# Performance work log

Measured on AMD Instinct MI355X. Metric: run time of the kernel, lower is better.

The kernel has to match this reference:

```python
import jax, jax.numpy as jnp
import numpy as np
from jax import lax

DIM = 256
NUM_HEADS = 8
HEAD_DIM = DIM // NUM_HEADS          # 32
KEY_DIM = int(HEAD_DIM * 0.5)        # 16
SCALE = KEY_DIM ** -0.5
H_QKV = DIM + KEY_DIM * NUM_HEADS * 2  # 512
BN_EPS = 1e-3  # keras BatchNormalization default epsilon


def conv_bn(x, w, gamma, beta, mean, var, groups=1):
    # Conv2D (no bias) + BatchNorm (inference), activation=None
    y = lax.conv_general_dilated(
        x, w, window_strides=(1, 1), padding='SAME',
        dimension_numbers=('NHWC', 'HWIO', 'NHWC'),
        feature_group_count=groups)
    return gamma * (y - mean) * lax.rsqrt(var + BN_EPS) + beta


def setup_inputs() -> dict:
    key = jax.random.key(0)
    ks = jax.random.split(key, 4)
    B, Hs, Ws = 8, 32, 32
    inp = {
        'inputs': jax.random.normal(ks[0], (B, Hs, Ws, DIM), dtype=jnp.float32),
        # qkv: 1x1 conv dim -> h
        'qkv_w': jax.random.normal(ks[1], (1, 1, DIM, H_QKV), dtype=jnp.float32) * 0.05,
        'qkv_gamma': jnp.ones((H_QKV,), jnp.float32),
        'qkv_beta': jnp.zeros((H_QKV,), jnp.float32),
        'qkv_mean': jnp.zeros((H_QKV,), jnp.float32),
        'qkv_var': jnp.ones((H_QKV,), jnp.float32),
        # pe: 3x3 depthwise conv (groups=dim)
        'pe_w': jax.random.normal(ks[2], (3, 3, 1, DIM), dtype=jnp.float32) * 0.05,
        'pe_gamma': jnp.ones((DIM,), jnp.float32),
        'pe_beta': jnp.zeros((DIM,), jnp.float32),
        'pe_mean': jnp.zeros((DIM,), jnp.float32),
        'pe_var': jnp.ones((DIM,), jnp.float32),
        # proj: 1x1 conv dim -> dim
        'proj_w': jax.random.normal(ks[3], (1, 1, DIM, DIM), dtype=jnp.float32) * 0.05,
        'proj_gamma': jnp.ones((DIM,), jnp.float32),
        'proj_beta': jnp.zeros((DIM,), jnp.float32),
        'proj_mean': jnp.zeros((DIM,), jnp.float32),
        'proj_var': jnp.ones((DIM,), jnp.float32),
    }
    return inp


def reference(inputs, qkv_w, qkv_gamma, qkv_beta, qkv_mean, qkv_var,
              pe_w, pe_gamma, pe_beta, pe_mean, pe_var,
              proj_w, proj_gamma, proj_beta, proj_mean, proj_var):
    B, Hs, Ws, C = inputs.shape
    N = Hs * Ws
    x = conv_bn(inputs, qkv_w, qkv_gamma, qkv_beta, qkv_mean, qkv_var)  # [B,H,W,h]
    x = x.reshape(B, N, NUM_HEADS, 2 * KEY_DIM + HEAD_DIM)
    q = x[..., :KEY_DIM]                          # [B,N,nh,kd]
    k = x[..., KEY_DIM:2 * KEY_DIM]               # [B,N,nh,kd]
    v = x[..., 2 * KEY_DIM:]                      # [B,N,nh,hd]
    # attn = q^T @ k^T : [B,nh,N,N]
    attn = jnp.einsum('bnhk,bmhk->bhnm', q, k) * SCALE
    attn = jax.nn.softmax(attn, axis=-1)
    # x = v^T @ attn : [B,nh,hd,N]
    x = jnp.einsum('bnhd,bhnm->bhdm', v, attn)
    # faithful to source: transpose [0,2,1,3] -> [B,hd,nh,N], then reshape NHWC
    x = jnp.transpose(x, (0, 2, 1, 3)).reshape(B, Hs, Ws, C)
    pe = conv_bn(v.reshape(B, Hs, Ws, C), pe_w, pe_gamma, pe_beta, pe_mean, pe_var, groups=C)
    x = x + pe
    x = conv_bn(x, proj_w, proj_gamma, proj_beta, proj_mean, proj_var)
    return x
```

## Files before the change

### kernel.cpp

```cpp
#include <hip/hip_runtime.h>

typedef _Float16 h4 __attribute__((ext_vector_type(4)));
typedef _Float16 h8 __attribute__((ext_vector_type(8)));
typedef float    f4 __attribute__((ext_vector_type(4)));

#define QSCALE (0.25f * 1.44269504088896f)

__device__ __forceinline__ float ex2(float x){ return __builtin_amdgcn_exp2f(x); }

__global__ __launch_bounds__(256) void prep_k(
    const float* __restrict__ X,
    const float* __restrict__ qkvw, const float* __restrict__ qg, const float* __restrict__ qb,
    const float* __restrict__ qm,   const float* __restrict__ qv,
    const float* __restrict__ pew,  const float* __restrict__ pg, const float* __restrict__ pb,
    const float* __restrict__ pm,   const float* __restrict__ pv,
    const float* __restrict__ prw,  const float* __restrict__ prg, const float* __restrict__ prb,
    const float* __restrict__ prm,  const float* __restrict__ prv,
    _Float16* __restrict__ Xh, _Float16* __restrict__ Wqkv, float* __restrict__ bqkv,
    _Float16* __restrict__ Wproj, float* __restrict__ bproj,
    float* __restrict__ peW, float* __restrict__ peB)
{
  const int gid = blockIdx.x*256 + threadIdx.x;
  const int gsz = gridDim.x*256;
  for (int i = gid; i < 2097152/4; i += gsz){
    const float4 xv = ((const float4*)X)[i];
    h4 o; o[0]=(_Float16)xv.x; o[1]=(_Float16)xv.y; o[2]=(_Float16)xv.z; o[3]=(_Float16)xv.w;
    ((h4*)Xh)[i] = o;
  }
  for (int i = gid; i < 512*256; i += gsz){
    int o = i >> 8, c = i & 255;
    float s = qg[o] * rsqrtf(qv[o] + 1e-3f);
    Wqkv[i] = (_Float16)(qkvw[c*512 + o] * s);
  }
  for (int i = gid; i < 512; i += gsz){
    float s = qg[i] * rsqrtf(qv[i] + 1e-3f);
    bqkv[i] = qb[i] - qm[i]*s;
  }
  for (int i = gid; i < 256*256; i += gsz){
    int o = i >> 8, c = i & 255;
    float s = prg[o] * rsqrtf(prv[o] + 1e-3f);
    Wproj[i] = (_Float16)(prw[c*256 + o] * s);
  }
  for (int i = gid; i < 256; i += gsz){
    float s = prg[i] * rsqrtf(prv[i] + 1e-3f);
    bproj[i] = prb[i] - prm[i]*s;
  }
  for (int i = gid; i < 9*256; i += gsz){
    int c = i & 255;
    float s = pg[c] * rsqrtf(pv[c] + 1e-3f);
    peW[i] = pew[i] * s;
  }
  for (int i = gid; i < 256; i += gsz){
    float s = pg[i] * rsqrtf(pv[i] + 1e-3f);
    peB[i] = pb[i] - pm[i]*s;
  }
}

template<int EPI, int MT>
__global__ __launch_bounds__(256) void gemm_k(
    const _Float16* __restrict__ A, const _Float16* __restrict__ Bt,
    const float* __restrict__ bias,
    _Float16* __restrict__ Qh, _Float16* __restrict__ Kh, _Float16* __restrict__ Vh,
    float* __restrict__ Out)
{
  const int t = threadIdx.x, lane = t & 63, wv = t >> 6;
  const int l15 = lane & 15, q = lane >> 4;
  const int mb = (blockIdx.x*4 + wv) * (16*MT);
  const int n0 = blockIdx.y * 64;
  f4 acc[MT][4] = {};
  #pragma unroll
  for (int kk = 0; kk < 8; ++kk){
    h8 af[MT];
    #pragma unroll
    for (int mi = 0; mi < MT; ++mi)
      af[mi] = *(const h8*)(A + (size_t)(mb + mi*16 + l15)*256 + kk*32 + q*8);
    #pragma unroll
    for (int nj = 0; nj < 4; ++nj){
      h8 bf = *(const h8*)(Bt + (size_t)(n0 + nj*16 + l15)*256 + kk*32 + q*8);
      #pragma unroll
      for (int mi = 0; mi < MT; ++mi)
        acc[mi][nj] = __builtin_amdgcn_mfma_f32_16x16x32_f16(af[mi], bf, acc[mi][nj], 0,0,0);
    }
  }
  #pragma unroll
  for (int mi = 0; mi < MT; ++mi)
  #pragma unroll
  for (int nj = 0; nj < 4; ++nj){
    const int og = n0 + nj*16 + l15;
    const float bs = bias[og];
    #pragma unroll
    for (int r = 0; r < 4; ++r){
      const int mg = mb + mi*16 + q*4 + r;
      const float v = acc[mi][nj][r] + bs;
      if (EPI == 0){
        const int h = og >> 6, j = og & 63;
        const int b = mg >> 10, n = mg & 1023;
        const size_t bhn = (size_t)(b*8+h)*1024 + n;
        if (j < 16)      Qh[bhn*16 + j]      = (_Float16)(v * QSCALE);
        else if (j < 32) Kh[bhn*16 + (j-16)] = (_Float16)v;
        else             Vh[bhn*32 + (j-32)] = (_Float16)v;
      } else {
        Out[(size_t)mg*256 + og] = v;
      }
    }
  }
}

__global__ __launch_bounds__(256) void pass1_k(
    const _Float16* __restrict__ Qh, const _Float16* __restrict__ Kh,
    const _Float16* __restrict__ Vh, _Float16* __restrict__ Vs)
{
  const int t = threadIdx.x, lane = t & 63, wv = t >> 6;
  const int l15 = lane & 15, q = lane >> 4;
  const int bh = blockIdx.y;
  const int n0 = (blockIdx.x*4 + wv) * 32;
  const size_t qb = (size_t)bh*1024;
  const h4 af0 = *(const h4*)(Qh + (qb + n0 + l15)*16 + q*4);
  const h4 af1 = *(const h4*)(Qh + (qb + n0 + 16 + l15)*16 + q*4);
  f4 sm0 = {0.f,0.f,0.f,0.f}, sm1 = {0.f,0.f,0.f,0.f};
  const _Float16* kp = Kh + qb*16;
  #pragma unroll 4
  for (int mt = 0; mt < 64; ++mt){
    h4 bf = *(const h4*)(kp + mt*256 + l15*16 + q*4);
    f4 z = {0.f,0.f,0.f,0.f};
    f4 d0 = __builtin_amdgcn_mfma_f32_16x16x16f16(af0, bf, z, 0,0,0);
    f4 d1 = __builtin_amdgcn_mfma_f32_16x16x16f16(af1, bf, z, 0,0,0);
    #pragma unroll
    for (int r = 0; r < 4; ++r){ sm0[r] += ex2(d0[r]); sm1[r] += ex2(d1[r]); }
  }
  #pragma unroll
  for (int st = 1; st < 16; st <<= 1){
    #pragma unroll
    for (int r = 0; r < 4; ++r){
      sm0[r] += __shfl_xor(sm0[r], st, 64);
      sm1[r] += __shfl_xor(sm1[r], st, 64);
    }
  }
  f4 cv0, cv1;
  #pragma unroll
  for (int r = 0; r < 4; ++r){ cv0[r] = 1.0f/sm0[r]; cv1[r] = 1.0f/sm1[r]; }
  #pragma unroll
  for (int half = 0; half < 2; ++half){
    const int dd = l15 + half*16;
    h4 o0, o1;
    #pragma unroll
    for (int r = 0; r < 4; ++r){
      o0[r] = (_Float16)((float)Vh[(qb + n0 + q*4 + r)*32 + dd] * cv0[r]);
      o1[r] = (_Float16)((float)Vh[(qb + n0 + 16 + q*4 + r)*32 + dd] * cv1[r]);
    }
    *(h4*)(Vs + ((size_t)bh*32 + dd)*1024 + n0 + q*4)      = o0;
    *(h4*)(Vs + ((size_t)bh*32 + dd)*1024 + n0 + 16 + q*4) = o1;
  }
}

__global__ __launch_bounds__(256) void pass2_k(
    const _Float16* __restrict__ Qh, const _Float16* __restrict__ Kh,
    const _Float16* __restrict__ Vs, _Float16* __restrict__ X1h)
{
  __shared__ float Tt[4][32*33];
  const int t = threadIdx.x, lane = t & 63, wv = t >> 6;
  const int l15 = lane & 15, q = lane >> 4;
  const int bh = blockIdx.y;
  const int b  = bh >> 3, h = bh & 7;
  const int mb = (blockIdx.x*4 + wv) * 32;
  const size_t qb = (size_t)bh*1024;
  const h4 kf0 = *(const h4*)(Kh + (qb + mb + l15)*16 + q*4);
  const h4 kf1 = *(const h4*)(Kh + (qb + mb + 16 + l15)*16 + q*4);
  const _Float16* qp  = Qh + qb*16;
  const _Float16* vp0 = Vs + ((size_t)bh*32 + l15)*1024;
  const _Float16* vp1 = vp0 + 16*1024;
  f4 a00={0.f,0.f,0.f,0.f}, a01={0.f,0.f,0.f,0.f};
  f4 a10={0.f,0.f,0.f,0.f}, a11={0.f,0.f,0.f,0.f};
  #pragma unroll 2
  for (int nt = 0; nt < 1024; nt += 16){
    h4 qf = *(const h4*)(qp + (nt + l15)*16 + q*4);
    h4 b0 = *(const h4*)(vp0 + nt + q*4);
    h4 b1 = *(const h4*)(vp1 + nt + q*4);
    f4 z = {0.f,0.f,0.f,0.f};
    f4 s0 = __builtin_amdgcn_mfma_f32_16x16x16f16(qf, kf0, z, 0,0,0);
    f4 s1 = __builtin_amdgcn_mfma_f32_16x16x16f16(qf, kf1, z, 0,0,0);
    h4 p0, p1;
    #pragma unroll
    for (int r = 0; r < 4; ++r){ p0[r] = (_Float16)ex2(s0[r]); p1[r] = (_Float16)ex2(s1[r]); }
    a00 = __builtin_amdgcn_mfma_f32_16x16x16f16(p0, b0, a00, 0,0,0);
    a01 = __builtin_amdgcn_mfma_f32_16x16x16f16(p0, b1, a01, 0,0,0);
    a10 = __builtin_amdgcn_mfma_f32_16x16x16f16(p1, b0, a10, 0,0,0);
    a11 = __builtin_amdgcn_mfma_f32_16x16x16f16(p1, b1, a11, 0,0,0);
  }
  #pragma unroll
  for (int r = 0; r < 4; ++r){
    Tt[wv][(q*4 + r)*33      + l15]      = a00[r];
    Tt[wv][(q*4 + r)*33      + 16 + l15] = a01[r];
    Tt[wv][(16 + q*4 + r)*33 + l15]      = a10[r];
    Tt[wv][(16 + q*4 + r)*33 + 16 + l15] = a11[r];
  }
  __syncthreads();
  _Float16* xb = X1h + (size_t)b*262144 + (size_t)h*1024 + mb;
  const int mloc = lane & 31, dh = lane >> 5;
  #pragma unroll
  for (int r = 0; r < 16; ++r){
    const int d = r*2 + dh;
    xb[(size_t)d*8192 + mloc] = (_Float16)Tt[wv][mloc*33 + d];
  }
}

__global__ __launch_bounds__(256) void pe_add_k(
    const _Float16* __restrict__ Vh, const _Float16* __restrict__ X1h,
    const float* __restrict__ peW, const float* __restrict__ peB,
    _Float16* __restrict__ X2h)
{
  const int idx = blockIdx.x*256 + threadIdx.x;
  const int c = idx & 255;
  const int tok = idx >> 8;
  const int b = tok >> 10, n = tok & 1023;
  const int hs = n >> 5, ws = n & 31;
  const int h = c >> 5, d = c & 31;
  float acc = peB[c];
  const _Float16* vb = Vh + (size_t)(b*8 + h)*32768 + d;
  #pragma unroll
  for (int dy = 0; dy < 3; ++dy){
    const int y = hs + dy - 1;
    if ((unsigned)y < 32u){
      #pragma unroll
      for (int dx = 0; dx < 3; ++dx){
        const int x = ws + dx - 1;
        if ((unsigned)x < 32u)
          acc += peW[(dy*3+dx)*256 + c] * (float)vb[(size_t)(y*32 + x)*32];
      }
    }
  }
  X2h[idx] = (_Float16)((float)X1h[idx] + acc);
}

extern "C" void kernel_launch(void* const* d_in, const int* in_sizes, int n_in,
                              void* d_out, int out_size, void* d_ws, size_t ws_size,
                              hipStream_t stream)
{
  const float* X    = (const float*)d_in[0];
  const float* qkvw = (const float*)d_in[1];
  const float* qg   = (const float*)d_in[2];
  const float* qb   = (const float*)d_in[3];
  const float* qm   = (const float*)d_in[4];
  const float* qv   = (const float*)d_in[5];
  const float* pew  = (const float*)d_in[6];
  const float* pg   = (const float*)d_in[7];
  const float* pb   = (const float*)d_in[8];
  const float* pm   = (const float*)d_in[9];
  const float* pv   = (const float*)d_in[10];
  const float* prw  = (const float*)d_in[11];
  const float* prg  = (const float*)d_in[12];
  const float* prb  = (const float*)d_in[13];
  const float* prm  = (const float*)d_in[14];
  const float* prv  = (const float*)d_in[15];

  char* ws = (char*)d_ws;
  _Float16* Xh    = (_Float16*)(ws + 0);
  _Float16* X2h   = (_Float16*)(ws + 0);
  _Float16* Qh    = (_Float16*)(ws + 4194304);
  _Float16* Kh    = (_Float16*)(ws + 6291456);
  _Float16* Vh    = (_Float16*)(ws + 8388608);
  _Float16* Vs    = (_Float16*)(ws + 12582912);
  _Float16* X1h   = (_Float16*)(ws + 16777216);
  _Float16* Wqkv  = (_Float16*)(ws + 20971520);
  float*    bqkv  = (float*)   (ws + 21233664);
  _Float16* Wproj = (_Float16*)(ws + 21235712);
  float*    bproj = (float*)   (ws + 21366784);
  float*    peW   = (float*)   (ws + 21367808);
  float*    peB   = (float*)   (ws + 21377024);

  prep_k<<<256, 256, 0, stream>>>(X, qkvw, qg, qb, qm, qv, pew, pg, pb, pm, pv,
                                  prw, prg, prb, prm, prv,
                                  Xh, Wqkv, bqkv, Wproj, bproj, peW, peB);
  gemm_k<0,2><<<dim3(64, 8), 256, 0, stream>>>(Xh, Wqkv, bqkv, Qh, Kh, Vh, nullptr);
  pass1_k<<<dim3(8, 64), 256, 0, stream>>>(Qh, Kh, Vh, Vs);
  pass2_k<<<dim3(8, 64), 256, 0, stream>>>(Qh, Kh, Vs, X1h);
  pe_add_k<<<8192, 256, 0, stream>>>(Vh, X1h, peW, peB, X2h);
  gemm_k<1,1><<<dim3(128, 4), 256, 0, stream>>>(X2h, Wproj, bproj,
                                                nullptr, nullptr, nullptr, (float*)d_out);
}
```

Measured before the change: 181.8 us.

## Fuse input fp16 cast into QKV GEMM and halve per-wave tiles for more parallelism

Removes the separate fp32-to-fp16 conversion of the input from the prep kernel; the QKV GEMM now reads fp32 activations directly and converts them in registers. The attention passes and both GEMMs shrink their per-wave tiles from 32 to 16 rows (and the projection GEMM from 64 to 32 output columns), doubling grid sizes to fill more compute units. This cuts one full read and write of the input but reduces operand reuse, so key/V tiles are reloaded more often from cache.

```diff
diff --git a/kernel.cpp b/kernel.cpp
--- a/kernel.cpp
+++ b/kernel.cpp
@@ -9,24 +9,18 @@
 __device__ __forceinline__ float ex2(float x){ return __builtin_amdgcn_exp2f(x); }
 
 __global__ __launch_bounds__(256) void prep_k(
-    const float* __restrict__ X,
     const float* __restrict__ qkvw, const float* __restrict__ qg, const float* __restrict__ qb,
     const float* __restrict__ qm,   const float* __restrict__ qv,
     const float* __restrict__ pew,  const float* __restrict__ pg, const float* __restrict__ pb,
     const float* __restrict__ pm,   const float* __restrict__ pv,
     const float* __restrict__ prw,  const float* __restrict__ prg, const float* __restrict__ prb,
     const float* __restrict__ prm,  const float* __restrict__ prv,
-    _Float16* __restrict__ Xh, _Float16* __restrict__ Wqkv, float* __restrict__ bqkv,
+    _Float16* __restrict__ Wqkv, float* __restrict__ bqkv,
     _Float16* __restrict__ Wproj, float* __restrict__ bproj,
     float* __restrict__ peW, float* __restrict__ peB)
 {
   const int gid = blockIdx.x*256 + threadIdx.x;
   const int gsz = gridDim.x*256;
-  for (int i = gid; i < 2097152/4; i += gsz){
-    const float4 xv = ((const float4*)X)[i];
-    h4 o; o[0]=(_Float16)xv.x; o[1]=(_Float16)xv.y; o[2]=(_Float16)xv.z; o[3]=(_Float16)xv.w;
-    ((h4*)Xh)[i] = o;
-  }
   for (int i = gid; i < 512*256; i += gsz){
     int o = i >> 8, c = i & 255;
     float s = qg[o] * rsqrtf(qv[o] + 1e-3f);
@@ -56,52 +50,43 @@
   }
 }
 
-template<int EPI, int MT>
-__global__ __launch_bounds__(256) void gemm_k(
-    const _Float16* __restrict__ A, const _Float16* __restrict__ Bt,
+__global__ __launch_bounds__(256) void qkv_gemm_k(
+    const float* __restrict__ X, const _Float16* __restrict__ Wqkv,
     const float* __restrict__ bias,
-    _Float16* __restrict__ Qh, _Float16* __restrict__ Kh, _Float16* __restrict__ Vh,
-    float* __restrict__ Out)
-{
-  const int t = threadIdx.x, lane = t & 63, wv = t >> 6;
-  const int l15 = lane & 15, q = lane >> 4;
-  const int mb = (blockIdx.x*4 + wv) * (16*MT);
+    _Float16* __restrict__ Qh, _Float16* __restrict__ Kh, _Float16* __restrict__ Vh)
+{
+  const int t = threadIdx.x, lane = t & 63, wv = t >> 6;
+  const int l15 = lane & 15, q = lane >> 4;
+  const int mb = (blockIdx.x*4 + wv) * 16;
   const int n0 = blockIdx.y * 64;
-  f4 acc[MT][4] = {};
+  f4 acc[4] = {};
   #pragma unroll
   for (int kk = 0; kk < 8; ++kk){
-    h8 af[MT];
-    #pragma unroll
-    for (int mi = 0; mi < MT; ++mi)
-      af[mi] = *(const h8*)(A + (size_t)(mb + mi*16 + l15)*256 + kk*32 + q*8);
+    const float4 a0 = *(const float4*)(X + (size_t)(mb + l15)*256 + kk*32 + q*8);
+    const float4 a1 = *(const float4*)(X + (size_t)(mb + l15)*256 + kk*32 + q*8 + 4);
+    h8 af; af[0]=(_Float16)a0.x; af[1]=(_Float16)a0.y; af[2]=(_Float16)a0.z; af[3]=(_Float16)a0.w;
+           af[4]=(_Float16)a1.x; af[5]=(_Float16)a1.y; af[6]=(_Float16)a1.z; af[7]=(_Float16)a1.w;
     #pragma unroll
     for (int nj = 0; nj < 4; ++nj){
-      h8 bf = *(const h8*)(Bt + (size_t)(n0 + nj*16 + l15)*256 + kk*32 + q*8);
-      #pragma unroll
-      for (int mi = 0; mi < MT; ++mi)
-        acc[mi][nj] = __builtin_amdgcn_mfma_f32_16x16x32_f16(af[mi], bf, acc[mi][nj], 0,0,0);
-    }
-  }
-  #pragma unroll
-  for (int mi = 0; mi < MT; ++mi)
+      h8 bf = *(const h8*)(Wqkv + (size_t)(n0 + nj*16 + l15)*256 + kk*32 + q*8);
+      acc[nj] = __builtin_amdgcn_mfma_f32_16x16x32_f16(af, bf, acc[nj], 0,0,0);
+    }
+  }
   #pragma unroll
   for (int nj = 0; nj < 4; ++nj){
     const int og = n0 + nj*16 + l15;
+    const int j  = og & 63;
+    const int h  = og >> 6;
     const float bs = bias[og];
     #pragma unroll
     for (int r = 0; r < 4; ++r){
-      const int mg = mb + mi*16 + q*4 + r;
-      const float v = acc[mi][nj][r] + bs;
-      if (EPI == 0){
-        const int h = og >> 6, j = og & 63;
-        const int b = mg >> 10, n = mg & 1023;
-        const size_t bhn = (size_t)(b*8+h)*1024 + n;
-        if (j < 16)      Qh[bhn*16 + j]      = (_Float16)(v * QSCALE);
-        else if (j < 32) Kh[bhn*16 + (j-16)] = (_Float16)v;
-        else             Vh[bhn*32 + (j-32)] = (_Float16)v;
-      } else {
-        Out[(size_t)mg*256 + og] = v;
-      }
+      const int mg = mb + q*4 + r;
+      const int b = mg >> 10, n = mg & 1023;
+      const size_t bhn = (size_t)(b*8+h)*1024 + n;
+      const float v = acc[nj][r] + bs;
+      if (j < 16)      Qh[bhn*16 + j]      = (_Float16)(v * QSCALE);
+      else if (j < 32) Kh[bhn*16 + (j-16)] = (_Float16)v;
+      else             Vh[bhn*32 + (j-32)] = (_Float16)v;
     }
   }
 }
@@ -113,43 +98,35 @@
   const int t = threadIdx.x, lane = t & 63, wv = t >> 6;
   const int l15 = lane & 15, q = lane >> 4;
   const int bh = blockIdx.y;
-  const int n0 = (blockIdx.x*4 + wv) * 32;
+  const int n0 = (blockIdx.x*4 + wv) * 16;
   const size_t qb = (size_t)bh*1024;
-  const h4 af0 = *(const h4*)(Qh + (qb + n0 + l15)*16 + q*4);
-  const h4 af1 = *(const h4*)(Qh + (qb + n0 + 16 + l15)*16 + q*4);
-  f4 sm0 = {0.f,0.f,0.f,0.f}, sm1 = {0.f,0.f,0.f,0.f};
+  const h4 af = *(const h4*)(Qh + (qb + n0 + l15)*16 + q*4);
+  f4 sm = {0.f,0.f,0.f,0.f};
   const _Float16* kp = Kh + qb*16;
-  #pragma unroll 4
+  #pragma unroll 8
   for (int mt = 0; mt < 64; ++mt){
     h4 bf = *(const h4*)(kp + mt*256 + l15*16 + q*4);
     f4 z = {0.f,0.f,0.f,0.f};
-    f4 d0 = __builtin_amdgcn_mfma_f32_16x16x16f16(af0, bf, z, 0,0,0);
-    f4 d1 = __builtin_amdgcn_mfma_f32_16x16x16f16(af1, bf, z, 0,0,0);
-    #pragma unroll
-    for (int r = 0; r < 4; ++r){ sm0[r] += ex2(d0[r]); sm1[r] += ex2(d1[r]); }
+    f4 d = __builtin_amdgcn_mfma_f32_16x16x16f16(af, bf, z, 0,0,0);
+    #pragma unroll
+    for (int r = 0; r < 4; ++r) sm[r] += ex2(d[r]);
   }
   #pragma unroll
   for (int st = 1; st < 16; st <<= 1){
     #pragma unroll
-    for (int r = 0; r < 4; ++r){
-      sm0[r] += __shfl_xor(sm0[r], st, 64);
-      sm1[r] += __shfl_xor(sm1[r], st, 64);
-    }
-  }
-  f4 cv0, cv1;
-  #pragma unroll
-  for (int r = 0; r < 4; ++r){ cv0[r] = 1.0f/sm0[r]; cv1[r] = 1.0f/sm1[r]; }
+    for (int r = 0; r < 4; ++r) sm[r] += __shfl_xor(sm[r], st, 64);
+  }
+  f4 cv;
+  #pragma unroll
+  for (int r = 0; r < 4; ++r) cv[r] = 1.0f/sm[r];
   #pragma unroll
   for (int half = 0; half < 2; ++half){
     const int dd = l15 + half*16;
-    h4 o0, o1;
-    #pragma unroll
-    for (int r = 0; r < 4; ++r){
-      o0[r] = (_Float16)((float)Vh[(qb + n0 + q*4 + r)*32 + dd] * cv0[r]);
-      o1[r] = (_Float16)((float)Vh[(qb + n0 + 16 + q*4 + r)*32 + dd] * cv1[r]);
-    }
-    *(h4*)(Vs + ((size_t)bh*32 + dd)*1024 + n0 + q*4)      = o0;
-    *(h4*)(Vs + ((size_t)bh*32 + dd)*1024 + n0 + 16 + q*4) = o1;
+    h4 o;
+    #pragma unroll
+    for (int r = 0; r < 4; ++r)
+      o[r] = (_Float16)((float)Vh[(qb + n0 + q*4 + r)*32 + dd] * cv[r]);
+    *(h4*)(Vs + ((size_t)bh*32 + dd)*1024 + n0 + q*4) = o;
   }
 }
 
@@ -157,50 +134,42 @@
     const _Float16* __restrict__ Qh, const _Float16* __restrict__ Kh,
     const _Float16* __restrict__ Vs, _Float16* __restrict__ X1h)
 {
-  __shared__ float Tt[4][32*33];
+  __shared__ float Tt[4][16*33];
   const int t = threadIdx.x, lane = t & 63, wv = t >> 6;
   const int l15 = lane & 15, q = lane >> 4;
   const int bh = blockIdx.y;
   const int b  = bh >> 3, h = bh & 7;
-  const int mb = (blockIdx.x*4 + wv) * 32;
+  const int mb = (blockIdx.x*4 + wv) * 16;
   const size_t qb = (size_t)bh*1024;
-  const h4 kf0 = *(const h4*)(Kh + (qb + mb + l15)*16 + q*4);
-  const h4 kf1 = *(const h4*)(Kh + (qb + mb + 16 + l15)*16 + q*4);
+  const h4 kf = *(const h4*)(Kh + (qb + mb + l15)*16 + q*4);
   const _Float16* qp  = Qh + qb*16;
   const _Float16* vp0 = Vs + ((size_t)bh*32 + l15)*1024;
   const _Float16* vp1 = vp0 + 16*1024;
-  f4 a00={0.f,0.f,0.f,0.f}, a01={0.f,0.f,0.f,0.f};
-  f4 a10={0.f,0.f,0.f,0.f}, a11={0.f,0.f,0.f,0.f};
-  #pragma unroll 2
+  f4 a0 = {0.f,0.f,0.f,0.f}, a1 = {0.f,0.f,0.f,0.f};
+  #pragma unroll 4
   for (int nt = 0; nt < 1024; nt += 16){
     h4 qf = *(const h4*)(qp + (nt + l15)*16 + q*4);
     h4 b0 = *(const h4*)(vp0 + nt + q*4);
     h4 b1 = *(const h4*)(vp1 + nt + q*4);
     f4 z = {0.f,0.f,0.f,0.f};
-    f4 s0 = __builtin_amdgcn_mfma_f32_16x16x16f16(qf, kf0, z, 0,0,0);
-    f4 s1 = __builtin_amdgcn_mfma_f32_16x16x16f16(qf, kf1, z, 0,0,0);
-    h4 p0, p1;
-    #pragma unroll
-    for (int r = 0; r < 4; ++r){ p0[r] = (_Float16)ex2(s0[r]); p1[r] = (_Float16)ex2(s1[r]); }
-    a00 = __builtin_amdgcn_mfma_f32_16x16x16f16(p0, b0, a00, 0,0,0);
-    a01 = __builtin_amdgcn_mfma_f32_16x16x16f16(p0, b1, a01, 0,0,0);
-    a10 = __builtin_amdgcn_mfma_f32_16x16x16f16(p1, b0, a10, 0,0,0);
-    a11 = __builtin_amdgcn_mfma_f32_16x16x16f16(p1, b1, a11, 0,0,0);
+    f4 s = __builtin_amdgcn_mfma_f32_16x16x16f16(qf, kf, z, 0,0,0);
+    h4 p;
+    #pragma unroll
+    for (int r = 0; r < 4; ++r) p[r] = (_Float16)ex2(s[r]);
+    a0 = __builtin_amdgcn_mfma_f32_16x16x16f16(p, b0, a0, 0,0,0);
+    a1 = __builtin_amdgcn_mfma_f32_16x16x16f16(p, b1, a1, 0,0,0);
   }
   #pragma unroll
   for (int r = 0; r < 4; ++r){
-    Tt[wv][(q*4 + r)*33      + l15]      = a00[r];
-    Tt[wv][(q*4 + r)*33      + 16 + l15] = a01[r];
-    Tt[wv][(16 + q*4 + r)*33 + l15]      = a10[r];
-    Tt[wv][(16 + q*4 + r)*33 + 16 + l15] = a11[r];
+    Tt[wv][(q*4 + r)*33 + l15]      = a0[r];
+    Tt[wv][(q*4 + r)*33 + 16 + l15] = a1[r];
   }
   __syncthreads();
   _Float16* xb = X1h + (size_t)b*262144 + (size_t)h*1024 + mb;
-  const int mloc = lane & 31, dh = lane >> 5;
-  #pragma unroll
-  for (int r = 0; r < 16; ++r){
-    const int d = r*2 + dh;
-    xb[(size_t)d*8192 + mloc] = (_Float16)Tt[wv][mloc*33 + d];
+  #pragma unroll
+  for (int r = 0; r < 8; ++r){
+    const int d = r*4 + q;
+    xb[(size_t)d*8192 + l15] = (_Float16)Tt[wv][l15*33 + d];
   }
 }
 
@@ -230,6 +199,36 @@
     }
   }
   X2h[idx] = (_Float16)((float)X1h[idx] + acc);
+}
+
+__global__ __launch_bounds__(256) void proj_gemm_k(
+    const _Float16* __restrict__ A, const _Float16* __restrict__ Wproj,
+    const float* __restrict__ bias, float* __restrict__ Out)
+{
+  const int t = threadIdx.x, lane = t & 63, wv = t >> 6;
+  const int l15 = lane & 15, q = lane >> 4;
+  const int mb = (blockIdx.x*4 + wv) * 16;
+  const int n0 = blockIdx.y * 32;
+  f4 acc[2] = {};
+  #pragma unroll
+  for (int kk = 0; kk < 8; ++kk){
+    h8 af = *(const h8*)(A + (size_t)(mb + l15)*256 + kk*32 + q*8);
+    #pragma unroll
+    for (int nj = 0; nj < 2; ++nj){
+      h8 bf = *(const h8*)(Wproj + (size_t)(n0 + nj*16 + l15)*256 + kk*32 + q*8);
+      acc[nj] = __builtin_amdgcn_mfma_f32_16x16x32_f16(af, bf, acc[nj], 0,0,0);
+    }
+  }
+  #pragma unroll
+  for (int nj = 0; nj < 2; ++nj){
+    const int og = n0 + nj*16 + l15;
+    const float bs = bias[og];
+    #pragma unroll
+    for (int r = 0; r < 4; ++r){
+      const int mg = mb + q*4 + r;
+      Out[(size_t)mg*256 + og] = acc[nj][r] + bs;
+    }
+  }
 }
 
 extern "C" void kernel_launch(void* const* d_in, const int* in_sizes, int n_in,
@@ -254,7 +253,6 @@
   const float* prv  = (const float*)d_in[15];
 
   char* ws = (char*)d_ws;
-  _Float16* Xh    = (_Float16*)(ws + 0);
   _Float16* X2h   = (_Float16*)(ws + 0);
   _Float16* Qh    = (_Float16*)(ws + 4194304);
   _Float16* Kh    = (_Float16*)(ws + 6291456);
@@ -268,13 +266,12 @@
   float*    peW   = (float*)   (ws + 21367808);
   float*    peB   = (float*)   (ws + 21377024);
 
-  prep_k<<<256, 256, 0, stream>>>(X, qkvw, qg, qb, qm, qv, pew, pg, pb, pm, pv,
+  prep_k<<<128, 256, 0, stream>>>(qkvw, qg, qb, qm, qv, pew, pg, pb, pm, pv,
                                   prw, prg, prb, prm, prv,
-                                  Xh, Wqkv, bqkv, Wproj, bproj, peW, peB);
-  gemm_k<0,2><<<dim3(64, 8), 256, 0, stream>>>(Xh, Wqkv, bqkv, Qh, Kh, Vh, nullptr);
-  pass1_k<<<dim3(8, 64), 256, 0, stream>>>(Qh, Kh, Vh, Vs);
-  pass2_k<<<dim3(8, 64), 256, 0, stream>>>(Qh, Kh, Vs, X1h);
+                                  Wqkv, bqkv, Wproj, bproj, peW, peB);
+  qkv_gemm_k<<<dim3(128, 8), 256, 0, stream>>>(X, Wqkv, bqkv, Qh, Kh, Vh);
+  pass1_k<<<dim3(16, 64), 256, 0, stream>>>(Qh, Kh, Vh, Vs);
+  pass2_k<<<dim3(16, 64), 256, 0, stream>>>(Qh, Kh, Vs, X1h);
   pe_add_k<<<8192, 256, 0, stream>>>(Vh, X1h, peW, peB, X2h);
-  gemm_k<1,1><<<dim3(128, 4), 256, 0, stream>>>(X2h, Wproj, bproj,
-                                                nullptr, nullptr, nullptr, (float*)d_out);
-}
+  proj_gemm_k<<<dim3(128, 8), 256, 0, stream>>>(X2h, Wproj, bproj, (float*)d_out);
+}
```

After: 218.7 us. 1.2x slower.
